# Performance work log

Measured on AMD Instinct MI355X. Metric: run time of the kernel, lower is better.

The kernel has to match this reference:

```python
import jax, jax.numpy as jnp
import numpy as np

NUM_USER = 50000
NUM_ITEM = 30000
N_NODES = NUM_USER + NUM_ITEM
N_EDGES = 1_000_000
FEAT_DIM = 768
DIM_LATENT = 128
DIM_ID = 64
NEG_SLOPE = 0.01  # F.leaky_relu default


def leaky_relu(x):
    return jnp.where(x >= 0, x, NEG_SLOPE * x)


def l2_normalize(x, eps=1e-12):
    # F.normalize(dim=-1): divide by clamped L2 norm
    n = jnp.sqrt(jnp.sum(x * x, axis=-1, keepdims=True))
    return x / jnp.maximum(n, eps)


def graph_gat(x, W, edge_index, num_nodes):
    """MGAT GraphGAT: x -> x@W, gated inner-product attention, softmax over
    incoming edges per destination node, scatter-add, L2 normalize."""
    x = x @ W                                    # [N, D]
    src = edge_index[0]                          # j (source)
    dst = edge_index[1]                          # i (target)
    x_j = x[src]                                 # [E, D]
    x_i = x[dst]                                 # [E, D]
    inner = jnp.sum(x_i * x_j, axis=-1)          # [E]
    # gate: sigmoid(deg(src)^-0.5 * inner)
    deg = jax.ops.segment_sum(jnp.ones_like(inner), src, num_segments=num_nodes)
    gate = jax.nn.sigmoid(deg[src] ** -0.5 * inner)
    score = inner * gate                         # [E]
    # segment softmax over destination nodes
    smax = jax.ops.segment_max(score, dst, num_segments=num_nodes)
    e = jnp.exp(score - smax[dst])
    denom = jax.ops.segment_sum(e, dst, num_segments=num_nodes)
    alpha = e / (denom[dst] + 1e-16)             # [E]
    out = jax.ops.segment_sum(x_j * alpha[:, None], dst, num_segments=num_nodes)
    return l2_normalize(out)


def setup_inputs() -> dict:
    key = jax.random.key(0)
    ks = jax.random.split(key, 16)

    def xavier(k, shape):
        fan_in, fan_out = shape[0], shape[1]
        std = float(np.sqrt(2.0 / (fan_in + fan_out)))
        return jax.random.normal(k, shape, dtype=jnp.float32) * std

    features = jax.random.normal(ks[0], (NUM_ITEM, FEAT_DIM), dtype=jnp.float32)
    id_embedding = jax.random.normal(ks[1], (N_NODES, DIM_ID), dtype=jnp.float32)
    # edge_index [2, E] with no self-loops (remove_self_loops is then identity)
    src = jax.random.randint(ks[2], (N_EDGES,), 0, N_NODES)
    off = jax.random.randint(ks[3], (N_EDGES,), 1, N_NODES)
    dst = (src + off) % N_NODES
    edge_index = jnp.stack([src, dst]).astype(jnp.int64)

    return {
        "features": features,
        "id_embedding": id_embedding,
        "edge_index": edge_index,
        "preference": xavier(ks[4], (NUM_USER, DIM_LATENT)),
        "mlp_w": xavier(ks[5], (FEAT_DIM, DIM_LATENT)),
        "mlp_b": jnp.zeros((DIM_LATENT,), dtype=jnp.float32),
        "conv1_w": xavier(ks[6], (DIM_LATENT, DIM_LATENT)),
        "lin1_w": xavier(ks[7], (DIM_LATENT, DIM_ID)),
        "lin1_b": jnp.zeros((DIM_ID,), dtype=jnp.float32),
        "g1_w": xavier(ks[8], (DIM_LATENT, DIM_ID)),
        "g1_b": jnp.zeros((DIM_ID,), dtype=jnp.float32),
        "conv2_w": xavier(ks[9], (DIM_ID, DIM_ID)),
        "lin2_w": xavier(ks[10], (DIM_ID, DIM_ID)),
        "lin2_b": jnp.zeros((DIM_ID,), dtype=jnp.float32),
        "g2_w": xavier(ks[11], (DIM_ID, DIM_ID)),
        "g2_b": jnp.zeros((DIM_ID,), dtype=jnp.float32),
    }


def reference(features, id_embedding, edge_index, preference, mlp_w, mlp_b,
              conv1_w, lin1_w, lin1_b, g1_w, g1_b,
              conv2_w, lin2_w, lin2_b, g2_w, g2_b):
    temp_features = jnp.tanh(features @ mlp_w + mlp_b)        # [num_item, dim_latent]
    x = jnp.concatenate([preference, temp_features], axis=0)  # [N, dim_latent]
    x = l2_normalize(x)

    h = leaky_relu(graph_gat(x, conv1_w, edge_index, N_NODES))
    x_hat = leaky_relu(x @ lin1_w + lin1_b) + id_embedding
    x1 = leaky_relu(h @ g1_w + g1_b + x_hat)                  # [N, dim_id]

    h = leaky_relu(graph_gat(x1, conv2_w, edge_index, N_NODES))
    x_hat = leaky_relu(x1 @ lin2_w + lin2_b) + id_embedding
    x2 = leaky_relu(h @ g2_w + g2_b + x_hat)                  # [N, dim_id]

    return jnp.concatenate([x1, x2], axis=1)                  # [N, 2*dim_id]
```

## Files before the change

kernel.cpp:

```cpp
#include <hip/hip_runtime.h>
#include <hip/hip_bf16.h>
#include <math.h>

#define NUM_USER 50000
#define NUM_ITEM 30000
#define N_NODES  80000
#define N_EDGES  1000000
#define FEAT_DIM 768
#define DLAT 128
#define DID  64
#define NEG_SLOPE 0.01f

#define SCAN_NB ((N_NODES + 255) / 256)
#define NB_COUNT ((N_EDGES + 255) / 256)
#define NB_WT 560
#define NB_MLP ((NUM_ITEM + 63) / 64)
#define NB_NORM (N_NODES / 8)
#define NB_CONV1 (N_NODES / 64)

__device__ __forceinline__ float leaky(float v) { return v >= 0.f ? v : NEG_SLOPE * v; }

__device__ __forceinline__ float wave_reduce_sum(float v) {
#pragma unroll
    for (int off = 32; off > 0; off >>= 1) v += __shfl_xor(v, off, 64);
    return v;
}

__device__ __forceinline__ unsigned short f2bf(float f) {
    unsigned int u = __float_as_uint(f);
    unsigned int r = u + 0x7fffu + ((u >> 16) & 1u);
    return (unsigned short)(r >> 16);
}
__device__ __forceinline__ float bf2f(unsigned short h) {
    return __uint_as_float(((unsigned int)h) << 16);
}

typedef __attribute__((ext_vector_type(8))) short short8v;
typedef __attribute__((ext_vector_type(4))) float f32x4;

__device__ __forceinline__ void unpack8(int4 v, float* f) {
    unsigned int u;
    u = (unsigned int)v.x; f[0] = __uint_as_float(u << 16); f[1] = __uint_as_float(u & 0xFFFF0000u);
    u = (unsigned int)v.y; f[2] = __uint_as_float(u << 16); f[3] = __uint_as_float(u & 0xFFFF0000u);
    u = (unsigned int)v.z; f[4] = __uint_as_float(u << 16); f[5] = __uint_as_float(u & 0xFFFF0000u);
    u = (unsigned int)v.w; f[6] = __uint_as_float(u << 16); f[7] = __uint_as_float(u & 0xFFFF0000u);
}

__device__ __forceinline__ void split_store8(
    float4 a, float4 b, unsigned short* dh, unsigned short* dl)
{
    float v[8] = {a.x, a.y, a.z, a.w, b.x, b.y, b.z, b.w};
    unsigned int ph[4], pl[4];
#pragma unroll
    for (int i = 0; i < 4; i++) {
        unsigned short h0 = f2bf(v[2*i]),   l0 = f2bf(v[2*i]   - bf2f(h0));
        unsigned short h1 = f2bf(v[2*i+1]), l1 = f2bf(v[2*i+1] - bf2f(h1));
        ph[i] = (unsigned int)h0 | ((unsigned int)h1 << 16);
        pl[i] = (unsigned int)l0 | ((unsigned int)l1 << 16);
    }
    *(int4*)dh = make_int4((int)ph[0], (int)ph[1], (int)ph[2], (int)ph[3]);
    *(int4*)dl = make_int4((int)pl[0], (int)pl[1], (int)pl[2], (int)pl[3]);
}


__device__ __forceinline__ void prep_one(int id, const float* W, int KK, int NN,
                                         unsigned short* Wh, unsigned short* Wl)
{
    int n = id / KK, k = id - n * KK;
    float v = W[(size_t)k * NN + n];
    unsigned short h = f2bf(v);
    Wh[id] = h;
    Wl[id] = f2bf(v - bf2f(h));
}

__device__ void wt_prep_body(int pb,
    const float* mlp_w, const float* c1, const float* l1, const float* g1,
    const float* c2, const float* l2, const float* g2,
    unsigned short* mlpWh, unsigned short* mlpWl,
    unsigned short* wc1h, unsigned short* wc1l,
    unsigned short* wl1h, unsigned short* wl1l,
    unsigned short* wg1h, unsigned short* wg1l,
    unsigned short* wc2h, unsigned short* wc2l,
    unsigned short* wl2h, unsigned short* wl2l,
    unsigned short* wg2h, unsigned short* wg2l)
{
    int id = pb * 256 + threadIdx.x;
    if (id < 98304)       prep_one(id,          mlp_w, FEAT_DIM, DLAT, mlpWh, mlpWl);
    else if (id < 114688) prep_one(id - 98304,  c1, DLAT, DLAT, wc1h, wc1l);
    else if (id < 122880) prep_one(id - 114688, l1, DLAT, DID,  wl1h, wl1l);
    else if (id < 131072) prep_one(id - 122880, g1, DLAT, DID,  wg1h, wg1l);
    else if (id < 135168) prep_one(id - 131072, c2, DID,  DID,  wc2h, wc2l);
    else if (id < 139264) prep_one(id - 135168, l2, DID,  DID,  wl2h, wl2l);
    else if (id < 143360) prep_one(id - 139264, g2, DID,  DID,  wg2h, wg2l);
}

__device__ void count_body(int pb, const int* src, const int* dst,
                           int* deg_out, int* cnt_in)
{
    int e = pb * 256 + threadIdx.x;
    if (e < N_EDGES) {
        atomicAdd(&deg_out[src[e]], 1);
        atomicAdd(&cnt_in[dst[e]], 1);
    }
}

__device__ void scan_local_body(int pb, const int* cnt, int* rowptr, int* blocksum)
{
    __shared__ int wsum[4];
    int gid = pb * 256 + threadIdx.x;
    int lane = threadIdx.x & 63, w = threadIdx.x >> 6;
    int orig = (gid < N_NODES) ? cnt[gid] : 0;
    int v = orig;
#pragma unroll
    for (int off = 1; off < 64; off <<= 1) {
        int u = __shfl_up(v, off, 64);
        if (lane >= off) v += u;
    }
    if (lane == 63) wsum[w] = v;
    __syncthreads();
    int woff = 0;
#pragma unroll
    for (int i = 0; i < 4; i++) woff += (i < w) ? wsum[i] : 0;
    if (gid < N_NODES) rowptr[gid] = v - orig + woff;
    if (threadIdx.x == 255) blocksum[pb] = woff + v;
}

__device__ void scan_blocksums_body(int* blocksum)
{
    __shared__ int s[512];
    int t = threadIdx.x;
    int orig = (t < SCAN_NB) ? blocksum[t] : 0;
    s[t] = orig;
    __syncthreads();
    for (int off = 1; off < 512; off <<= 1) {
        int u = (t >= off) ? s[t - off] : 0;
        __syncthreads();
        s[t] += u;
        __syncthreads();
    }
    if (t < SCAN_NB) blocksum[t] = s[t] - orig;
}

__device__ void scan_add_plus_body(int pb, int* rowptr, const int* blocksum,
                                   int* cnt, const int* deg_out, float* rsq)
{
    int gid = pb * 256 + threadIdx.x;
    if (gid < N_NODES) {
        rowptr[gid] += blocksum[pb];
        cnt[gid] = 0;
        rsq[gid] = rsqrtf((float)deg_out[gid]);
    }
    if (gid == 0) rowptr[N_NODES] = N_EDGES;
}

__device__ void mlp_body(int pb, const float* F,
    const unsigned short* Wh, const unsigned short* Wl,
    const float* bias, float* xout)
{
    __shared__ unsigned short sAh[64][72];
    __shared__ unsigned short sAl[64][72];
    __shared__ unsigned short sWh[128][72];
    __shared__ unsigned short sWlo[128][72];

    const int tid = threadIdx.x;
    const int lane = tid & 63;
    const int w = tid >> 6;
    const int wr = w >> 1, wc = w & 1;
    const int r0 = pb * 64;

    f32x4 acc[2][4];
#pragma unroll
    for (int m = 0; m < 2; m++)
#pragma unroll
        for (int n = 0; n < 4; n++) acc[m][n] = (f32x4){0.f, 0.f, 0.f, 0.f};

    for (int kc = 0; kc < FEAT_DIM; kc += 64) {
#pragma unroll
        for (int it = 0; it < 2; it++) {
            int slot = tid + it * 256;
            int row = slot >> 3;
            int k8 = (slot & 7) * 8;
            int gr = r0 + row;
            float4 a = make_float4(0.f, 0.f, 0.f, 0.f), b = a;
            if (gr < NUM_ITEM) {
                const float4* p = (const float4*)(F + (size_t)gr * FEAT_DIM + kc + k8);
                a = p[0]; b = p[1];
            }
            split_store8(a, b, &sAh[row][k8], &sAl[row][k8]);
        }
#pragma unroll
        for (int it = 0; it < 4; it++) {
            int slot = tid + it * 256;
            int n = slot >> 3;
            int k8 = (slot & 7) * 8;
            *(int4*)&sWh[n][k8]  = *(const int4*)(Wh + (size_t)n * FEAT_DIM + kc + k8);
            *(int4*)&sWlo[n][k8] = *(const int4*)(Wl + (size_t)n * FEAT_DIM + kc + k8);
        }
        __syncthreads();

#pragma unroll
        for (int k0 = 0; k0 < 64; k0 += 32) {
            int klane = k0 + (lane >> 4) * 8;
            short8v ah[2], al[2], bh[4], bl[4];
#pragma unroll
            for (int m = 0; m < 2; m++) {
                int row = wr * 32 + m * 16 + (lane & 15);
                ah[m] = *(const short8v*)&sAh[row][klane];
                al[m] = *(const short8v*)&sAl[row][klane];
            }
#pragma unroll
            for (int n = 0; n < 4; n++) {
                int col = wc * 64 + n * 16 + (lane & 15);
                bh[n] = *(const short8v*)&sWh[col][klane];
                bl[n] = *(const short8v*)&sWlo[col][klane];
            }
#pragma unroll
            for (int m = 0; m < 2; m++)
#pragma unroll
                for (int n = 0; n < 4; n++) {
                    acc[m][n] = __builtin_amdgcn_mfma_f32_16x16x32_bf16(ah[m], bh[n], acc[m][n], 0, 0, 0);
                    acc[m][n] = __builtin_amdgcn_mfma_f32_16x16x32_bf16(ah[m], bl[n], acc[m][n], 0, 0, 0);
                    acc[m][n] = __builtin_amdgcn_mfma_f32_16x16x32_bf16(al[m], bh[n], acc[m][n], 0, 0, 0);
                }
        }
        __syncthreads();
    }

#pragma unroll
    for (int m = 0; m < 2; m++) {
        int rbase = r0 + wr * 32 + m * 16 + (lane >> 4) * 4;
#pragma unroll
        for (int n = 0; n < 4; n++) {
            int col = wc * 64 + n * 16 + (lane & 15);
            float bv = bias[col];
#pragma unroll
            for (int q = 0; q < 4; q++) {
                int gr = rbase + q;
                if (gr < NUM_ITEM)
                    xout[(size_t)gr * DLAT + col] = tanhf(acc[m][n][q] + bv);
            }
        }
    }
}

__device__ void normcopy_body(int pb, const float* pref, float* x)
{
    int wid = pb * 8 + (threadIdx.x >> 6);
    if (wid >= N_NODES) return;
    int lane = threadIdx.x & 63;
    const float* srow = (wid < NUM_USER) ? (pref + (size_t)wid * DLAT)
                                         : (x + (size_t)wid * DLAT);
    float v0 = srow[lane], v1 = srow[lane + 64];
    float s = wave_reduce_sum(v0 * v0 + v1 * v1);
    float inv = 1.0f / fmaxf(sqrtf(s), 1e-12f);
    float* drow = x + (size_t)wid * DLAT;
    drow[lane] = v0 * inv;
    drow[lane + 64] = v1 * inv;
}

template<int K, int NC>
__device__ void conv_body(int pb, const float* X, int ldx,
    const unsigned short* Wth, const unsigned short* Wtl,
    unsigned short* O, int ldo)
{
    constexpr int NW = NC / 64;
    constexpr int MW = 4 / NW;
    constexpr int WROWS = 64 / MW;
    constexpr int MF = WROWS / 16;
    constexpr int KSTEPS = K / 32;
    constexpr int KP = K + 8;

    __shared__ unsigned short sAh[64][KP];
    __shared__ unsigned short sAl[64][KP];

    const int tid = threadIdx.x;
    const int lane = tid & 63;
    const int w = tid >> 6;
    const int wr = w / NW, wc = w % NW;
    const int r0 = pb * 64;

#pragma unroll
    for (int it = 0; it < K / 32; it++) {
        int slot = tid + it * 256;
        int row = slot / (K / 8);
        int k8 = (slot % (K / 8)) * 8;
        const float4* p = (const float4*)(X + (size_t)(r0 + row) * ldx + k8);
        split_store8(p[0], p[1], &sAh[row][k8], &sAl[row][k8]);
    }
    __syncthreads();

    f32x4 acc[MF][4];
#pragma unroll
    for (int m = 0; m < MF; m++)
#pragma unroll
        for (int n = 0; n < 4; n++) acc[m][n] = (f32x4){0.f, 0.f, 0.f, 0.f};

#pragma unroll
    for (int ks = 0; ks < KSTEPS; ks++) {
        int klane = ks * 32 + (lane >> 4) * 8;
        short8v ah[MF], al[MF];
#pragma unroll
        for (int m = 0; m < MF; m++) {
            int row = wr * WROWS + m * 16 + (lane & 15);
            ah[m] = *(const short8v*)&sAh[row][klane];
            al[m] = *(const short8v*)&sAl[row][klane];
        }
#pragma unroll
        for (int n = 0; n < 4; n++) {
            int col = wc * 64 + n * 16 + (lane & 15);
            short8v bh = *(const short8v*)(Wth + (size_t)col * K + klane);
            short8v bl = *(const short8v*)(Wtl + (size_t)col * K + klane);
#pragma unroll
            for (int m = 0; m < MF; m++) {
                acc[m][n] = __builtin_amdgcn_mfma_f32_16x16x32_bf16(ah[m], bh, acc[m][n], 0, 0, 0);
                acc[m][n] = __builtin_amdgcn_mfma_f32_16x16x32_bf16(ah[m], bl, acc[m][n], 0, 0, 0);
                acc[m][n] = __builtin_amdgcn_mfma_f32_16x16x32_bf16(al[m], bh, acc[m][n], 0, 0, 0);
            }
        }
    }

#pragma unroll
    for (int m = 0; m < MF; m++) {
        int rbase = r0 + wr * WROWS + m * 16 + (lane >> 4) * 4;
#pragma unroll
        for (int n = 0; n < 4; n++) {
            int col = wc * 64 + n * 16 + (lane & 15);
#pragma unroll
            for (int q = 0; q < 4; q++)
                O[(size_t)(rbase + q) * ldo + col] = f2bf(acc[m][n][q]);
        }
    }
}


__global__ __launch_bounds__(256) void k_count_wtprep(
    const int* __restrict__ src, const int* __restrict__ dst,
    int* __restrict__ deg_out, int* __restrict__ cnt_in,
    const float* __restrict__ mlp_w, const float* __restrict__ c1,
    const float* __restrict__ l1, const float* __restrict__ g1,
    const float* __restrict__ c2, const float* __restrict__ l2,
    const float* __restrict__ g2,
    unsigned short* __restrict__ mlpWh, unsigned short* __restrict__ mlpWl,
    unsigned short* __restrict__ wc1h, unsigned short* __restrict__ wc1l,
    unsigned short* __restrict__ wl1h, unsigned short* __restrict__ wl1l,
    unsigned short* __restrict__ wg1h, unsigned short* __restrict__ wg1l,
    unsigned short* __restrict__ wc2h, unsigned short* __restrict__ wc2l,
    unsigned short* __restrict__ wl2h, unsigned short* __restrict__ wl2l,
    unsigned short* __restrict__ wg2h, unsigned short* __restrict__ wg2l)
{
    int b = blockIdx.x;
    if (b < NB_COUNT) count_body(b, src, dst, deg_out, cnt_in);
    else wt_prep_body(b - NB_COUNT, mlp_w, c1, l1, g1, c2, l2, g2,
                      mlpWh, mlpWl, wc1h, wc1l, wl1h, wl1l, wg1h, wg1l,
                      wc2h, wc2l, wl2h, wl2l, wg2h, wg2l);
}

__global__ __launch_bounds__(256) void k_scanl_mlp(
    const int* __restrict__ cnt, int* __restrict__ rowptr, int* __restrict__ blocksum,
    const float* __restrict__ F, const unsigned short* __restrict__ Wh,
    const unsigned short* __restrict__ Wl, const float* __restrict__ bias,
    float* __restrict__ xout)
{
    int b = blockIdx.x;
    if (b < SCAN_NB) scan_local_body(b, cnt, rowptr, blocksum);
    else mlp_body(b - SCAN_NB, F, Wh, Wl, bias, xout);
}

__global__ __launch_bounds__(512) void k_scanb_norm(
    int* __restrict__ blocksum, const float* __restrict__ pref, float* __restrict__ x)
{
    int b = blockIdx.x;
    if (b == 0) scan_blocksums_body(blocksum);
    else normcopy_body(b - 1, pref, x);
}

__global__ __launch_bounds__(256) void k_scana_conv1(
    int* __restrict__ rowptr, const int* __restrict__ blocksum,
    int* __restrict__ cnt, const int* __restrict__ deg_out, float* __restrict__ rsq,
    const float* __restrict__ X,
    const unsigned short* __restrict__ Wth, const unsigned short* __restrict__ Wtl,
    unsigned short* __restrict__ O)
{
    int b = blockIdx.x;
    if (b < SCAN_NB) scan_add_plus_body(b, rowptr, blocksum, cnt, deg_out, rsq);
    else conv_body<DLAT, DLAT>(b - SCAN_NB, X, DLAT, Wth, Wtl, O, DLAT);
}


__global__ __launch_bounds__(256) void csr_fill_kernel(
    const int* __restrict__ src, const int* __restrict__ dst,
    const int* __restrict__ rowptr, int* __restrict__ cursor, int* __restrict__ csr_src)
{
    int e = blockIdx.x * 256 + threadIdx.x;
    if (e < N_EDGES) {
        int d = dst[e];
        int slot = rowptr[d] + atomicAdd(&cursor[d], 1);
        csr_src[slot] = src[e];
    }
}

__global__ __launch_bounds__(256) void conv2_kernel(
    const float* __restrict__ X, int ldx,
    const unsigned short* __restrict__ Wth, const unsigned short* __restrict__ Wtl,
    unsigned short* __restrict__ O, int ldo)
{
    conv_body<DID, DID>(blockIdx.x, X, ldx, Wth, Wtl, O, ldo);
}

template<int D>
__global__ __launch_bounds__(256) void gat_layer_kernel(
    const unsigned short* __restrict__ xw, const int* __restrict__ rowptr,
    const int* __restrict__ csr_src, const float* __restrict__ rsq_deg,
    float* __restrict__ h)
{
    constexpr int SG  = D / 8;
    constexpr int EPC = 64 / SG;
    int wid = blockIdx.x * 4 + (threadIdx.x >> 6);
    if (wid >= N_NODES) return;
    const int lane = threadIdx.x & 63;
    const int g = lane / SG;
    const int t = lane % SG;
    const int start = rowptr[wid], end = rowptr[wid + 1];

    float xd[8];
    unpack8(*(const int4*)(xw + (size_t)wid * D + 8 * t), xd);

    float l = 0.f;
    float acc[8];
#pragma unroll
    for (int c = 0; c < 8; c++) acc[c] = 0.f;

    for (int base = start; base < end; base += EPC) {
        int i = base + g;
        bool valid = (i < end);
        int s = valid ? csr_src[i] : 0;
        float a[8];
        unpack8(*(const int4*)(xw + (size_t)s * D + 8 * t), a);
        float p = a[0]*xd[0] + a[1]*xd[1] + a[2]*xd[2] + a[3]*xd[3]
                + a[4]*xd[4] + a[5]*xd[5] + a[6]*xd[6] + a[7]*xd[7];
#pragma unroll
        for (int off = SG / 2; off > 0; off >>= 1) p += __shfl_xor(p, off, 64);
        float rsd = valid ? rsq_deg[s] : 1.f;
        float gate = 1.0f / (1.0f + __expf(-(p * rsd)));
        float sc = fminf(p * gate, 80.f);
        float w = valid ? __expf(sc) : 0.f;
        l += w;
#pragma unroll
        for (int c = 0; c < 8; c++) acc[c] += w * a[c];
    }

#pragma unroll
    for (int off = SG; off < 64; off <<= 1) {
        l += __shfl_xor(l, off, 64);
#pragma unroll
        for (int c = 0; c < 8; c++) acc[c] += __shfl_xor(acc[c], off, 64);
    }

    float invl = 1.0f / (l + 1e-16f);
    float ss = 0.f;
#pragma unroll
    for (int c = 0; c < 8; c++) { acc[c] *= invl; ss += acc[c] * acc[c]; }
#pragma unroll
    for (int off = SG / 2; off > 0; off >>= 1) ss += __shfl_xor(ss, off, 64);
    float inv = 1.0f / fmaxf(sqrtf(ss), 1e-12f);

    if (g == 0) {
        float4 o0, o1;
        o0.x = leaky(acc[0] * inv); o0.y = leaky(acc[1] * inv);
        o0.z = leaky(acc[2] * inv); o0.w = leaky(acc[3] * inv);
        o1.x = leaky(acc[4] * inv); o1.y = leaky(acc[5] * inv);
        o1.z = leaky(acc[6] * inv); o1.w = leaky(acc[7] * inv);
        float* op = h + (size_t)wid * D + 8 * t;
        *(float4*)(op) = o0;
        *(float4*)(op + 4) = o1;
    }
}

template<int K>
__global__ __launch_bounds__(256) void combine_mfma_kernel(
    const float* __restrict__ H, int ldh,
    const float* __restrict__ X, int ldx,
    const unsigned short* __restrict__ Gth, const unsigned short* __restrict__ Gtl,
    const unsigned short* __restrict__ Lth, const unsigned short* __restrict__ Ltl,
    const float* __restrict__ g_b, const float* __restrict__ lin_b,
    const float* __restrict__ id_emb, float* __restrict__ out, int out_off)
{
    constexpr int KSTEPS = K / 32;
    constexpr int KP = K + 8;

    __shared__ unsigned short sHh[64][KP];
    __shared__ unsigned short sHl[64][KP];
    __shared__ unsigned short sXh[64][KP];
    __shared__ unsigned short sXl[64][KP];

    const int tid = threadIdx.x;
    const int lane = tid & 63;
    const int wr = tid >> 6;
    const int r0 = blockIdx.x * 64;

#pragma unroll
    for (int it = 0; it < K / 32; it++) {
        int slot = tid + it * 256;
        int row = slot / (K / 8);
        int k8 = (slot % (K / 8)) * 8;
        const float4* ph = (const float4*)(H + (size_t)(r0 + row) * ldh + k8);
        split_store8(ph[0], ph[1], &sHh[row][k8], &sHl[row][k8]);
        const float4* px = (const float4*)(X + (size_t)(r0 + row) * ldx + k8);
        split_store8(px[0], px[1], &sXh[row][k8], &sXl[row][k8]);
    }
    __syncthreads();

    f32x4 accG[4], accL[4];
#pragma unroll
    for (int n = 0; n < 4; n++) {
        accG[n] = (f32x4){0.f, 0.f, 0.f, 0.f};
        accL[n] = (f32x4){0.f, 0.f, 0.f, 0.f};
    }

#pragma unroll
    for (int ks = 0; ks < KSTEPS; ks++) {
        int klane = ks * 32 + (lane >> 4) * 8;
        int row = wr * 16 + (lane & 15);
        short8v hh = *(const short8v*)&sHh[row][klane];
        short8v hl = *(const short8v*)&sHl[row][klane];
        short8v xh = *(const short8v*)&sXh[row][klane];
        short8v xl = *(const short8v*)&sXl[row][klane];
#pragma unroll
        for (int n = 0; n < 4; n++) {
            int col = n * 16 + (lane & 15);
            short8v gh = *(const short8v*)(Gth + (size_t)col * K + klane);
            short8v gl = *(const short8v*)(Gtl + (size_t)col * K + klane);
            short8v lh = *(const short8v*)(Lth + (size_t)col * K + klane);
            short8v ll = *(const short8v*)(Ltl + (size_t)col * K + klane);
            accG[n] = __builtin_amdgcn_mfma_f32_16x16x32_bf16(hh, gh, accG[n], 0, 0, 0);
            accG[n] = __builtin_amdgcn_mfma_f32_16x16x32_bf16(hh, gl, accG[n], 0, 0, 0);
            accG[n] = __builtin_amdgcn_mfma_f32_16x16x32_bf16(hl, gh, accG[n], 0, 0, 0);
            accL[n] = __builtin_amdgcn_mfma_f32_16x16x32_bf16(xh, lh, accL[n], 0, 0, 0);
            accL[n] = __builtin_amdgcn_mfma_f32_16x16x32_bf16(xh, ll, accL[n], 0, 0, 0);
            accL[n] = __builtin_amdgcn_mfma_f32_16x16x32_bf16(xl, lh, accL[n], 0, 0, 0);
        }
    }

    int rbase = r0 + wr * 16 + (lane >> 4) * 4;
#pragma unroll
    for (int n = 0; n < 4; n++) {
        int col = n * 16 + (lane & 15);
        float gb = g_b[col], lb = lin_b[col];
#pragma unroll
        for (int q = 0; q < 4; q++) {
            int gr = rbase + q;
            float xhv = leaky(accL[n][q] + lb) + id_emb[(size_t)gr * DID + col];
            float v = leaky(accG[n][q] + gb + xhv);
            out[(size_t)gr * (2 * DID) + out_off + col] = v;
        }
    }
}

extern "C" void kernel_launch(void* const* d_in, const int* in_sizes, int n_in,
                              void* d_out, int out_size, void* d_ws, size_t ws_size,
                              hipStream_t stream)
{
    const float* features = (const float*)d_in[0];
    const float* id_emb   = (const float*)d_in[1];
    const int*   ei       = (const int*)d_in[2];
    const float* pref     = (const float*)d_in[3];
    const float* mlp_w    = (const float*)d_in[4];
    const float* mlp_b    = (const float*)d_in[5];
    const float* conv1_w  = (const float*)d_in[6];
    const float* lin1_w   = (const float*)d_in[7];
    const float* lin1_b   = (const float*)d_in[8];
    const float* g1_w     = (const float*)d_in[9];
    const float* g1_b     = (const float*)d_in[10];
    const float* conv2_w  = (const float*)d_in[11];
    const float* lin2_w   = (const float*)d_in[12];
    const float* lin2_b   = (const float*)d_in[13];
    const float* g2_w     = (const float*)d_in[14];
    const float* g2_b     = (const float*)d_in[15];
    const int* src = ei;
    const int* dst = ei + N_EDGES;
    float* out = (float*)d_out;

    float* x        = (float*)d_ws;
    unsigned short* xwb = (unsigned short*)(x + (size_t)N_NODES * DLAT);
    float* gat      = (float*)(xwb + (size_t)N_NODES * DLAT);
    int*   deg_out  = (int*)(gat + (size_t)N_NODES * DLAT);
    int*   cnt      = deg_out + N_NODES;
    int*   rowptr   = cnt + N_NODES;
    int*   csr_src  = rowptr + N_NODES + 1;
    int*   blocksum = csr_src + N_EDGES;
    float* rsq_deg  = (float*)(blocksum + SCAN_NB);
    unsigned short* mlpWh = (unsigned short*)gat;
    unsigned short* mlpWl = mlpWh + (size_t)FEAT_DIM * DLAT;
    unsigned short* wbase = (unsigned short*)(
        (((uintptr_t)(rsq_deg + N_NODES)) + 15) & ~(uintptr_t)15);
    unsigned short* wc1h = wbase;
    unsigned short* wc1l = wc1h + 16384;
    unsigned short* wl1h = wc1l + 16384;
    unsigned short* wl1l = wl1h + 8192;
    unsigned short* wg1h = wl1l + 8192;
    unsigned short* wg1l = wg1h + 8192;
    unsigned short* wc2h = wg1l + 8192;
    unsigned short* wc2l = wc2h + 4096;
    unsigned short* wl2h = wc2l + 4096;
    unsigned short* wl2l = wl2h + 4096;
    unsigned short* wg2h = wl2l + 4096;
    unsigned short* wg2l = wg2h + 4096;

    hipMemsetAsync(deg_out, 0, 2 * N_NODES * sizeof(int), stream);

    k_count_wtprep<<<NB_COUNT + NB_WT, 256, 0, stream>>>(
        src, dst, deg_out, cnt,
        mlp_w, conv1_w, lin1_w, g1_w, conv2_w, lin2_w, g2_w,
        mlpWh, mlpWl, wc1h, wc1l, wl1h, wl1l, wg1h, wg1l,
        wc2h, wc2l, wl2h, wl2l, wg2h, wg2l);

    k_scanl_mlp<<<SCAN_NB + NB_MLP, 256, 0, stream>>>(
        cnt, rowptr, blocksum, features, mlpWh, mlpWl, mlp_b,
        x + (size_t)NUM_USER * DLAT);

    k_scanb_norm<<<1 + NB_NORM, 512, 0, stream>>>(blocksum, pref, x);

    k_scana_conv1<<<SCAN_NB + NB_CONV1, 256, 0, stream>>>(
        rowptr, blocksum, cnt, deg_out, rsq_deg, x, wc1h, wc1l, xwb);

    csr_fill_kernel<<<NB_COUNT, 256, 0, stream>>>(src, dst, rowptr, cnt, csr_src);

    gat_layer_kernel<DLAT><<<(N_NODES + 3) / 4, 256, 0, stream>>>(
        xwb, rowptr, csr_src, rsq_deg, gat);
    combine_mfma_kernel<DLAT><<<N_NODES / 64, 256, 0, stream>>>(
        gat, DLAT, x, DLAT, wg1h, wg1l, wl1h, wl1l, g1_b, lin1_b, id_emb, out, 0);

    conv2_kernel<<<N_NODES / 64, 256, 0, stream>>>(out, 2 * DID, wc2h, wc2l, xwb, DID);
    gat_layer_kernel<DID><<<(N_NODES + 3) / 4, 256, 0, stream>>>(
        xwb, rowptr, csr_src, rsq_deg, gat);
    combine_mfma_kernel<DID><<<N_NODES / 64, 256, 0, stream>>>(
        gat, DID, out, 2 * DID, wg2h, wg2l, wl2h, wl2l, g2_b, lin2_b, id_emb, out, DID);
}
```

Measured before the change: 452.7 us.

## Re-partition preprocessing kernels to overlap edge counting with MLP and conv1

Splits the edge-count pass into in-degree and out-degree parts. The in-degree atomics are interleaved with the MLP GEMM blocks, and the out-degree atomics with the conv1 GEMM blocks, so that atomic-bound and compute-bound work share the GPU. The block-sum scan becomes a single-wave shuffle scan, and the CSR cursor is initialised to the row start so the fill kernel no longer reads rowptr. This adds one extra kernel launch for weight prep and one for the scan-add, and its correctness depends on the hardcoded group counts (1304, 9:1 and 3:1 interleaves).

```diff
diff --git a/kernel.cpp b/kernel.cpp
--- a/kernel.cpp
+++ b/kernel.cpp
@@ -15,7 +15,7 @@
 #define NB_COUNT ((N_EDGES + 255) / 256)
 #define NB_WT 560
 #define NB_MLP ((NUM_ITEM + 63) / 64)
-#define NB_NORM (N_NODES / 8)
+#define NB_NORM4 (N_NODES / 4)
 #define NB_CONV1 (N_NODES / 64)
 
 __device__ __forceinline__ float leaky(float v) { return v >= 0.f ? v : NEG_SLOPE * v; }
@@ -73,18 +73,20 @@
     Wl[id] = f2bf(v - bf2f(h));
 }
 
-__device__ void wt_prep_body(int pb,
-    const float* mlp_w, const float* c1, const float* l1, const float* g1,
-    const float* c2, const float* l2, const float* g2,
-    unsigned short* mlpWh, unsigned short* mlpWl,
-    unsigned short* wc1h, unsigned short* wc1l,
-    unsigned short* wl1h, unsigned short* wl1l,
-    unsigned short* wg1h, unsigned short* wg1l,
-    unsigned short* wc2h, unsigned short* wc2l,
-    unsigned short* wl2h, unsigned short* wl2l,
-    unsigned short* wg2h, unsigned short* wg2l)
-{
-    int id = pb * 256 + threadIdx.x;
+__global__ __launch_bounds__(256) void wt_prep_kernel(
+    const float* __restrict__ mlp_w, const float* __restrict__ c1,
+    const float* __restrict__ l1, const float* __restrict__ g1,
+    const float* __restrict__ c2, const float* __restrict__ l2,
+    const float* __restrict__ g2,
+    unsigned short* __restrict__ mlpWh, unsigned short* __restrict__ mlpWl,
+    unsigned short* __restrict__ wc1h, unsigned short* __restrict__ wc1l,
+    unsigned short* __restrict__ wl1h, unsigned short* __restrict__ wl1l,
+    unsigned short* __restrict__ wg1h, unsigned short* __restrict__ wg1l,
+    unsigned short* __restrict__ wc2h, unsigned short* __restrict__ wc2l,
+    unsigned short* __restrict__ wl2h, unsigned short* __restrict__ wl2l,
+    unsigned short* __restrict__ wg2h, unsigned short* __restrict__ wg2l)
+{
+    int id = blockIdx.x * 256 + threadIdx.x;
     if (id < 98304)       prep_one(id,          mlp_w, FEAT_DIM, DLAT, mlpWh, mlpWl);
     else if (id < 114688) prep_one(id - 98304,  c1, DLAT, DLAT, wc1h, wc1l);
     else if (id < 122880) prep_one(id - 114688, l1, DLAT, DID,  wl1h, wl1l);
@@ -94,14 +96,16 @@
     else if (id < 143360) prep_one(id - 139264, g2, DID,  DID,  wg2h, wg2l);
 }
 
-__device__ void count_body(int pb, const int* src, const int* dst,
-                           int* deg_out, int* cnt_in)
+__device__ void count_in_body(int pb, const int* dst, int* cnt_in)
 {
     int e = pb * 256 + threadIdx.x;
-    if (e < N_EDGES) {
-        atomicAdd(&deg_out[src[e]], 1);
-        atomicAdd(&cnt_in[dst[e]], 1);
-    }
+    if (e < N_EDGES) atomicAdd(&cnt_in[dst[e]], 1);
+}
+
+__device__ void count_out_body(int pb, const int* src, int* deg_out)
+{
+    int e = pb * 256 + threadIdx.x;
+    if (e < N_EDGES) atomicAdd(&deg_out[src[e]], 1);
 }
 
 __device__ void scan_local_body(int pb, const int* cnt, int* rowptr, int* blocksum)
@@ -125,32 +129,33 @@
     if (threadIdx.x == 255) blocksum[pb] = woff + v;
 }
 
-__device__ void scan_blocksums_body(int* blocksum)
-{
-    __shared__ int s[512];
-    int t = threadIdx.x;
-    int orig = (t < SCAN_NB) ? blocksum[t] : 0;
-    s[t] = orig;
-    __syncthreads();
-    for (int off = 1; off < 512; off <<= 1) {
-        int u = (t >= off) ? s[t - off] : 0;
-        __syncthreads();
-        s[t] += u;
-        __syncthreads();
-    }
-    if (t < SCAN_NB) blocksum[t] = s[t] - orig;
-}
-
-__device__ void scan_add_plus_body(int pb, int* rowptr, const int* blocksum,
-                                   int* cnt, const int* deg_out, float* rsq)
-{
-    int gid = pb * 256 + threadIdx.x;
-    if (gid < N_NODES) {
-        rowptr[gid] += blocksum[pb];
-        cnt[gid] = 0;
-        rsq[gid] = rsqrtf((float)deg_out[gid]);
-    }
-    if (gid == 0) rowptr[N_NODES] = N_EDGES;
+__device__ void scan_blocksums_wave_body(int* blocksum)
+{
+    if (threadIdx.x >= 64) return;
+    int lane = threadIdx.x;
+    const int PER = (SCAN_NB + 63) / 64;
+    int vals[PER];
+    int s = 0;
+#pragma unroll
+    for (int i = 0; i < PER; i++) {
+        int idx = lane * PER + i;
+        vals[i] = (idx < SCAN_NB) ? blocksum[idx] : 0;
+        s += vals[i];
+    }
+    int incl = s;
+#pragma unroll
+    for (int off = 1; off < 64; off <<= 1) {
+        int u = __shfl_up(incl, off, 64);
+        if (lane >= off) incl += u;
+    }
+    int run = incl - s;
+#pragma unroll
+    for (int i = 0; i < PER; i++) {
+        int idx = lane * PER + i;
+        int v = vals[i];
+        if (idx < SCAN_NB) blocksum[idx] = run;
+        run += v;
+    }
 }
 
 __device__ void mlp_body(int pb, const float* F,
@@ -245,7 +250,7 @@
 
 __device__ void normcopy_body(int pb, const float* pref, float* x)
 {
-    int wid = pb * 8 + (threadIdx.x >> 6);
+    int wid = pb * 4 + (threadIdx.x >> 6);
     if (wid >= N_NODES) return;
     int lane = threadIdx.x & 63;
     const float* srow = (wid < NUM_USER) ? (pref + (size_t)wid * DLAT)
@@ -333,68 +338,73 @@
 }
 
 
-__global__ __launch_bounds__(256) void k_count_wtprep(
-    const int* __restrict__ src, const int* __restrict__ dst,
-    int* __restrict__ deg_out, int* __restrict__ cnt_in,
-    const float* __restrict__ mlp_w, const float* __restrict__ c1,
-    const float* __restrict__ l1, const float* __restrict__ g1,
-    const float* __restrict__ c2, const float* __restrict__ l2,
-    const float* __restrict__ g2,
-    unsigned short* __restrict__ mlpWh, unsigned short* __restrict__ mlpWl,
-    unsigned short* __restrict__ wc1h, unsigned short* __restrict__ wc1l,
-    unsigned short* __restrict__ wl1h, unsigned short* __restrict__ wl1l,
-    unsigned short* __restrict__ wg1h, unsigned short* __restrict__ wg1l,
-    unsigned short* __restrict__ wc2h, unsigned short* __restrict__ wc2l,
-    unsigned short* __restrict__ wl2h, unsigned short* __restrict__ wl2l,
-    unsigned short* __restrict__ wg2h, unsigned short* __restrict__ wg2l)
-{
-    int b = blockIdx.x;
-    if (b < NB_COUNT) count_body(b, src, dst, deg_out, cnt_in);
-    else wt_prep_body(b - NB_COUNT, mlp_w, c1, l1, g1, c2, l2, g2,
-                      mlpWh, mlpWl, wc1h, wc1l, wl1h, wl1l, wg1h, wg1l,
-                      wc2h, wc2l, wl2h, wl2l, wg2h, wg2l);
-}
-
-__global__ __launch_bounds__(256) void k_scanl_mlp(
-    const int* __restrict__ cnt, int* __restrict__ rowptr, int* __restrict__ blocksum,
+__global__ __launch_bounds__(256) void k_countin_mlp(
+    const int* __restrict__ dst, int* __restrict__ cnt_in,
     const float* __restrict__ F, const unsigned short* __restrict__ Wh,
     const unsigned short* __restrict__ Wl, const float* __restrict__ bias,
     float* __restrict__ xout)
 {
     int b = blockIdx.x;
+    int grp = b / 10, rem = b - grp * 10;
+    if (rem < 9) {
+        int cb = grp * 9 + rem;
+        if (cb < NB_COUNT) count_in_body(cb, dst, cnt_in);
+    } else {
+        if (grp < NB_MLP) mlp_body(grp, F, Wh, Wl, bias, xout);
+    }
+}
+
+__global__ __launch_bounds__(256) void k_scanl_norm(
+    const int* __restrict__ cnt, int* __restrict__ rowptr, int* __restrict__ blocksum,
+    const float* __restrict__ pref, float* __restrict__ x)
+{
+    int b = blockIdx.x;
     if (b < SCAN_NB) scan_local_body(b, cnt, rowptr, blocksum);
-    else mlp_body(b - SCAN_NB, F, Wh, Wl, bias, xout);
-}
-
-__global__ __launch_bounds__(512) void k_scanb_norm(
-    int* __restrict__ blocksum, const float* __restrict__ pref, float* __restrict__ x)
-{
-    int b = blockIdx.x;
-    if (b == 0) scan_blocksums_body(blocksum);
-    else normcopy_body(b - 1, pref, x);
-}
-
-__global__ __launch_bounds__(256) void k_scana_conv1(
-    int* __restrict__ rowptr, const int* __restrict__ blocksum,
-    int* __restrict__ cnt, const int* __restrict__ deg_out, float* __restrict__ rsq,
+    else normcopy_body(b - SCAN_NB, pref, x);
+}
+
+__global__ __launch_bounds__(256) void k_countout_conv1_scanb(
+    const int* __restrict__ src, int* __restrict__ deg_out,
     const float* __restrict__ X,
     const unsigned short* __restrict__ Wth, const unsigned short* __restrict__ Wtl,
-    unsigned short* __restrict__ O)
+    unsigned short* __restrict__ O, int* __restrict__ blocksum)
 {
     int b = blockIdx.x;
-    if (b < SCAN_NB) scan_add_plus_body(b, rowptr, blocksum, cnt, deg_out, rsq);
-    else conv_body<DLAT, DLAT>(b - SCAN_NB, X, DLAT, Wth, Wtl, O, DLAT);
-}
-
+    const int NGRP = 1304;
+    if (b < NGRP * 4) {
+        int grp = b >> 2, rem = b & 3;
+        if (rem < 3) {
+            int cb = grp * 3 + rem;
+            if (cb < NB_COUNT) count_out_body(cb, src, deg_out);
+        } else {
+            if (grp < NB_CONV1) conv_body<DLAT, DLAT>(grp, X, DLAT, Wth, Wtl, O, DLAT);
+        }
+    } else {
+        scan_blocksums_wave_body(blocksum);
+    }
+}
+
+__global__ __launch_bounds__(256) void scan_add_plus_kernel(
+    int* __restrict__ rowptr, const int* __restrict__ blocksum,
+    int* __restrict__ cursor, const int* __restrict__ deg_out, float* __restrict__ rsq)
+{
+    int gid = blockIdx.x * 256 + threadIdx.x;
+    if (gid < N_NODES) {
+        int r = rowptr[gid] + blocksum[blockIdx.x];
+        rowptr[gid] = r;
+        cursor[gid] = r;
+        rsq[gid] = rsqrtf((float)deg_out[gid]);
+    }
+    if (gid == 0) rowptr[N_NODES] = N_EDGES;
+}
 
 __global__ __launch_bounds__(256) void csr_fill_kernel(
     const int* __restrict__ src, const int* __restrict__ dst,
-    const int* __restrict__ rowptr, int* __restrict__ cursor, int* __restrict__ csr_src)
+    int* __restrict__ cursor, int* __restrict__ csr_src)
 {
     int e = blockIdx.x * 256 + threadIdx.x;
     if (e < N_EDGES) {
-        int d = dst[e];
-        int slot = rowptr[d] + atomicAdd(&cursor[d], 1);
+        int slot = atomicAdd(&cursor[dst[e]], 1);
         csr_src[slot] = src[e];
     }
 }
@@ -608,22 +618,24 @@
 
     hipMemsetAsync(deg_out, 0, 2 * N_NODES * sizeof(int), stream);
 
-    k_count_wtprep<<<NB_COUNT + NB_WT, 256, 0, stream>>>(
-        src, dst, deg_out, cnt,
+    wt_prep_kernel<<<NB_WT, 256, 0, stream>>>(
         mlp_w, conv1_w, lin1_w, g1_w, conv2_w, lin2_w, g2_w,
         mlpWh, mlpWl, wc1h, wc1l, wl1h, wl1l, wg1h, wg1l,
         wc2h, wc2l, wl2h, wl2l, wg2h, wg2l);
 
-    k_scanl_mlp<<<SCAN_NB + NB_MLP, 256, 0, stream>>>(
-        cnt, rowptr, blocksum, features, mlpWh, mlpWl, mlp_b,
-        x + (size_t)NUM_USER * DLAT);
-
-    k_scanb_norm<<<1 + NB_NORM, 512, 0, stream>>>(blocksum, pref, x);
-
-    k_scana_conv1<<<SCAN_NB + NB_CONV1, 256, 0, stream>>>(
-        rowptr, blocksum, cnt, deg_out, rsq_deg, x, wc1h, wc1l, xwb);
-
-    csr_fill_kernel<<<NB_COUNT, 256, 0, stream>>>(src, dst, rowptr, cnt, csr_src);
+    k_countin_mlp<<<NB_MLP * 10, 256, 0, stream>>>(
+        dst, cnt, features, mlpWh, mlpWl, mlp_b, x + (size_t)NUM_USER * DLAT);
+
+    k_scanl_norm<<<SCAN_NB + NB_NORM4, 256, 0, stream>>>(
+        cnt, rowptr, blocksum, pref, x);
+
+    k_countout_conv1_scanb<<<1304 * 4 + 1, 256, 0, stream>>>(
+        src, deg_out, x, wc1h, wc1l, xwb, blocksum);
+
+    scan_add_plus_kernel<<<SCAN_NB, 256, 0, stream>>>(
+        rowptr, blocksum, cnt, deg_out, rsq_deg);
+
+    csr_fill_kernel<<<NB_COUNT, 256, 0, stream>>>(src, dst, cnt, csr_src);
 
     gat_layer_kernel<DLAT><<<(N_NODES + 3) / 4, 256, 0, stream>>>(
         xwb, rowptr, csr_src, rsq_deg, gat);
```

New measurement: 529.0 us. 16.9% more time.
